# Kernel optimization log

Hardware: AMD Instinct MI355X
Metric: run time of the kernel (lower is better)

Reference implementation:

```python
import jax, jax.numpy as jnp
import numpy as np

# Tree: 64 leaves (16 feat -> 16 out), 8 mids (16 feat + 8*16 child = 144 -> 32 out),
# root (16 feat + 8*32 child = 272 -> 64 out), head -> 10 tasks. Eval-mode BatchNorm.
B = 16384
EPS = 1e-5


def setup_inputs() -> dict:
    key = jax.random.key(0)
    ks = jax.random.split(key, 24)
    rn = lambda k, s: jax.random.normal(k, s, dtype=jnp.float32)
    ru = lambda k, s: jax.random.uniform(k, s, dtype=jnp.float32)
    return {
        "x": rn(ks[0], (B, 1168)),
        # leaf layers (64 nodes, 16 -> 16)
        "Wl": rn(ks[1], (64, 16, 16)) * 0.1, "bl": rn(ks[2], (64, 16)) * 0.1,
        "gl": ru(ks[3], (64, 16)) + 0.5, "betal": rn(ks[4], (64, 16)) * 0.1,
        "ml": rn(ks[5], (64, 16)) * 0.1, "vl": ru(ks[6], (64, 16)) + 0.5,
        # mid layers (8 nodes, 144 -> 32)
        "Wm": rn(ks[7], (8, 144, 32)) * 0.1, "bm": rn(ks[8], (8, 32)) * 0.1,
        "gm": ru(ks[9], (8, 32)) + 0.5, "betam": rn(ks[10], (8, 32)) * 0.1,
        "mm": rn(ks[11], (8, 32)) * 0.1, "vm": ru(ks[12], (8, 32)) + 0.5,
        # root layer (272 -> 64)
        "Wr": rn(ks[13], (272, 64)) * 0.1, "br": rn(ks[14], (64,)) * 0.1,
        "gr": ru(ks[15], (64,)) + 0.5, "betar": rn(ks[16], (64,)) * 0.1,
        "mr": rn(ks[17], (64,)) * 0.1, "vr": ru(ks[18], (64,)) + 0.5,
        # root prediction head (64 -> 10 tasks)
        "Wh": rn(ks[19], (64, 10)) * 0.1, "bh": rn(ks[20], (10,)) * 0.1,
    }


def _bn(h, g, b, m, v):
    return (h - m) * jax.lax.rsqrt(v + EPS) * g + b


def reference(x, Wl, bl, gl, betal, ml, vl, Wm, bm, gm, betam, mm, vm,
              Wr, br, gr, betar, mr, vr, Wh, bh):
    n = x.shape[0]
    # leaves: gather own features (contiguous layout), Linear+BN+Tanh, batched over 64 nodes
    xl = x[:, :1024].reshape(n, 64, 16)
    hl = jnp.tanh(_bn(jnp.einsum('bli,lio->blo', xl, Wl) + bl, gl, betal, ml, vl))
    # mids: concat own features with 8 leaf-child outputs -> [n, 8, 144]
    xm = x[:, 1024:1152].reshape(n, 8, 16)
    mid_in = jnp.concatenate([xm, hl.reshape(n, 8, 128)], axis=-1)
    hm = jnp.tanh(_bn(jnp.einsum('bmi,mio->bmo', mid_in, Wm) + bm, gm, betam, mm, vm))
    # root: concat own features with 8 mid outputs -> [n, 272]
    root_in = jnp.concatenate([x[:, 1152:1168], hm.reshape(n, 256)], axis=-1)
    hr = jnp.tanh(_bn(root_in @ Wr + br, gr, betar, mr, vr))
    # root prediction head (eval-mode forward returns only root prediction)
    return hr @ Wh + bh
```

## Files before the change

kernel.cpp:

```cpp
#include <hip/hip_runtime.h>

typedef __attribute__((ext_vector_type(8))) short bf16x8;
typedef __attribute__((ext_vector_type(4))) float f32x4;

#define EPS 1e-5f

#define N_FRAG_BLOCKS 182
#define WSB_LEAF 0
#define WSB_MID  64
#define WSB_ROOT 144
#define WSB_HEAD 180
#define ST_SL 0
#define ST_TL 1024
#define ST_SM 2048
#define ST_TM 2304
#define ST_SR 2560
#define ST_TR 2624
#define WS_ST_BYTE_OFF (N_FRAG_BLOCKS * 1024)

__device__ __forceinline__ unsigned short f2bf(float f) {
    unsigned u = __float_as_uint(f);
    unsigned r = u + 0x7fffu + ((u >> 16) & 1u);
    return (unsigned short)(r >> 16);
}

__device__ __forceinline__ unsigned pack2bf(float a, float b) {
    return (unsigned)f2bf(a) | ((unsigned)f2bf(b) << 16);
}

__device__ __forceinline__ bf16x8 pack8(float4 a, float4 b) {
    union { unsigned u[4]; bf16x8 v; } r;
    r.u[0] = pack2bf(a.x, a.y); r.u[1] = pack2bf(a.z, a.w);
    r.u[2] = pack2bf(b.x, b.y); r.u[3] = pack2bf(b.z, b.w);
    return r.v;
}

__device__ __forceinline__ float tanh_fast(float x) {
    float e = __expf(2.0f * x);
    return 1.0f - 2.0f / (e + 1.0f);
}

__global__ void ontology_prep(
    const float* __restrict__ Wl, const float* __restrict__ Wm,
    const float* __restrict__ Wr, const float* __restrict__ Wh,
    const float* __restrict__ bl, const float* __restrict__ gl,
    const float* __restrict__ betal, const float* __restrict__ ml,
    const float* __restrict__ vl,
    const float* __restrict__ bm, const float* __restrict__ gm,
    const float* __restrict__ betam, const float* __restrict__ mm,
    const float* __restrict__ vm,
    const float* __restrict__ br, const float* __restrict__ gr,
    const float* __restrict__ betar, const float* __restrict__ mr,
    const float* __restrict__ vr,
    unsigned short* __restrict__ wsFrag, float* __restrict__ wsST)
{
    const int b = blockIdx.x;
    const int t = threadIdx.x;
    if (b < N_FRAG_BLOCKS) {
        const int row = t & 15, g = t >> 4;
        unsigned short vals[8];
        #pragma unroll
        for (int i = 0; i < 8; ++i) {
            const int k = g * 8 + i;
            float v = 0.f;
            if (b < 64) {
                const int l = b;
                if ((l & 1) == 0) { if (k < 16)  v = Wl[l * 256 + k * 16 + row]; }
                else              { if (k >= 16) v = Wl[l * 256 + (k - 16) * 16 + row]; }
            } else if (b < 144) {
                const int idx = b - 64, m = idx / 10, rem = idx % 10;
                const int tt = rem / 5, s = rem % 5;
                const int krow = s * 32 + k;
                if (krow < 144) v = Wm[m * 4608 + krow * 32 + tt * 16 + row];
            } else if (b < 180) {
                const int idx = b - 144, tt = idx / 9, s = idx % 9;
                if (s == 0) { if (k < 16) v = Wr[k * 64 + tt * 16 + row]; }
                else { const int krow = 16 + (s - 1) * 32 + k;
                       v = Wr[krow * 64 + tt * 16 + row]; }
            } else {
                const int s = b - 180, krow = s * 32 + k;
                if (row < 10) v = Wh[krow * 10 + row];
            }
            vals[i] = f2bf(v);
        }
        #pragma unroll
        for (int i = 0; i < 8; ++i) wsFrag[b * 512 + t * 8 + i] = vals[i];
    } else if (b == N_FRAG_BLOCKS) {
        for (int i = 0; i < 16; ++i) {
            const int id = t + 64 * i;
            const float S = gl[id] * rsqrtf(vl[id] + EPS);
            wsST[ST_SL + id] = S;
            wsST[ST_TL + id] = (bl[id] - ml[id]) * S + betal[id];
        }
    } else if (b == N_FRAG_BLOCKS + 1) {
        for (int i = 0; i < 4; ++i) {
            const int id = t + 64 * i;
            const float S = gm[id] * rsqrtf(vm[id] + EPS);
            wsST[ST_SM + id] = S;
            wsST[ST_TM + id] = (bm[id] - mm[id]) * S + betam[id];
        }
    } else {
        const int id = t;
        const float S = gr[id] * rsqrtf(vr[id] + EPS);
        wsST[ST_SR + id] = S;
        wsST[ST_TR + id] = (br[id] - mr[id]) * S + betar[id];
    }
}

__global__ __launch_bounds__(256, 4) void ontology_mfma(
    const float* __restrict__ x,
    const unsigned short* __restrict__ wsFrag,
    const float* __restrict__ wsST,
    const float* __restrict__ bh,
    float* __restrict__ out)
{
    __shared__ __align__(16) unsigned short mid_in[4][16][168];
    __shared__ __align__(16) unsigned short hm[16][264];
    unsigned short (*hr)[72] = (unsigned short (*)[72])&mid_in[0][0][0];

    const int w    = threadIdx.x >> 6;
    const int lane = threadIdx.x & 63;
    const int c    = lane & 15;
    const int g    = lane >> 4;
    const int rowbase = blockIdx.x * 16;
    const float* xrow = x + (size_t)(rowbase + c) * 1168;
    const int m0 = 2 * w, m1 = 2 * w + 1;

    float4 xr_a = *(const float4*)(xrow + 1152 + (g & 1) * 8);
    float4 xr_b = *(const float4*)(xrow + 1152 + (g & 1) * 8 + 4);
    float4 xm4_0 = *(const float4*)(xrow + 1024 + m0 * 16 + 4 * g);
    float4 xm4_1 = *(const float4*)(xrow + 1024 + m1 * 16 + 4 * g);
    float4 xp0[4][2], xp1[4][2];
    #pragma unroll
    for (int p = 0; p < 4; ++p) {
        const float* a0 = xrow + (m0 * 4 + p) * 32 + g * 8;
        xp0[p][0] = *(const float4*)a0;
        xp0[p][1] = *(const float4*)(a0 + 4);
    }
    #pragma unroll
    for (int p = 0; p < 4; ++p) {
        const float* a1 = xrow + (m1 * 4 + p) * 32 + g * 8;
        xp1[p][0] = *(const float4*)a1;
        xp1[p][1] = *(const float4*)(a1 + 4);
    }

    const float* Sl = wsST + ST_SL; const float* Tl = wsST + ST_TL;
    const float* Sm = wsST + ST_SM; const float* Tm = wsST + ST_TM;
    const float* Sr = wsST + ST_SR; const float* Tr = wsST + ST_TR;

    {
        uint2 z; z.x = 0u; z.y = 0u;
        *(uint2*)&mid_in[w][c][144 + 4 * g] = z;
    }

    f32x4 accR;
    {
        bf16x8 bfrag = pack8(xr_a, xr_b);
        bf16x8 a = *(const bf16x8*)(wsFrag + (WSB_ROOT + w * 9) * 512 + lane * 8);
        f32x4 zz = {0.f, 0.f, 0.f, 0.f};
        accR = __builtin_amdgcn_mfma_f32_16x16x32_bf16(a, bfrag, zz, 0, 0, 0);
    }

    auto phase = [&](int mi, const float4& xm4, const float4 xp[4][2]) {
        {
            uint2 pm; pm.x = pack2bf(xm4.x, xm4.y); pm.y = pack2bf(xm4.z, xm4.w);
            *(uint2*)&mid_in[w][c][4 * g] = pm;
        }
        #pragma unroll
        for (int p = 0; p < 4; ++p) {
            bf16x8 bfrag = pack8(xp[p][0], xp[p][1]);
            #pragma unroll
            for (int e = 0; e < 2; ++e) {
                const int leaf = mi * 8 + p * 2 + e;
                bf16x8 afrag = *(const bf16x8*)(wsFrag + (WSB_LEAF + leaf) * 512 + lane * 8);
                f32x4 zz = {0.f, 0.f, 0.f, 0.f};
                f32x4 acc = __builtin_amdgcn_mfma_f32_16x16x32_bf16(afrag, bfrag, zz, 0, 0, 0);
                float4 S = *(const float4*)(Sl + leaf * 16 + 4 * g);
                float4 T = *(const float4*)(Tl + leaf * 16 + 4 * g);
                float h0 = tanh_fast(acc[0] * S.x + T.x);
                float h1 = tanh_fast(acc[1] * S.y + T.y);
                float h2 = tanh_fast(acc[2] * S.z + T.z);
                float h3 = tanh_fast(acc[3] * S.w + T.w);
                uint2 pk; pk.x = pack2bf(h0, h1); pk.y = pack2bf(h2, h3);
                *(uint2*)&mid_in[w][c][16 + (p * 2 + e) * 16 + 4 * g] = pk;
            }
        }
        {
            f32x4 acc0 = {0.f, 0.f, 0.f, 0.f};
            f32x4 acc1 = {0.f, 0.f, 0.f, 0.f};
            const unsigned short* fb = wsFrag + (WSB_MID + mi * 10) * 512 + lane * 8;
            #pragma unroll
            for (int s = 0; s < 5; ++s) {
                bf16x8 bfrag = *(const bf16x8*)&mid_in[w][c][s * 32 + g * 8];
                bf16x8 a0 = *(const bf16x8*)(fb + s * 512);
                bf16x8 a1 = *(const bf16x8*)(fb + (5 + s) * 512);
                acc0 = __builtin_amdgcn_mfma_f32_16x16x32_bf16(a0, bfrag, acc0, 0, 0, 0);
                acc1 = __builtin_amdgcn_mfma_f32_16x16x32_bf16(a1, bfrag, acc1, 0, 0, 0);
            }
            #pragma unroll
            for (int t = 0; t < 2; ++t) {
                f32x4 acc = t ? acc1 : acc0;
                const int po = mi * 32 + t * 16 + 4 * g;
                float4 S = *(const float4*)(Sm + po);
                float4 T = *(const float4*)(Tm + po);
                float h0 = tanh_fast(acc[0] * S.x + T.x);
                float h1 = tanh_fast(acc[1] * S.y + T.y);
                float h2 = tanh_fast(acc[2] * S.z + T.z);
                float h3 = tanh_fast(acc[3] * S.w + T.w);
                uint2 pk; pk.x = pack2bf(h0, h1); pk.y = pack2bf(h2, h3);
                *(uint2*)&hm[c][po] = pk;
            }
        }
    };

    phase(m0, xm4_0, xp0);
    phase(m1, xm4_1, xp1);

    __syncthreads();

    {
        const unsigned short* fb = wsFrag + (WSB_ROOT + w * 9) * 512 + lane * 8;
        #pragma unroll
        for (int s = 1; s <= 8; ++s) {
            bf16x8 bfrag = *(const bf16x8*)&hm[c][(s - 1) * 32 + g * 8];
            bf16x8 a0 = *(const bf16x8*)(fb + s * 512);
            accR = __builtin_amdgcn_mfma_f32_16x16x32_bf16(a0, bfrag, accR, 0, 0, 0);
        }
        const int po = w * 16 + 4 * g;
        float4 S = *(const float4*)(Sr + po);
        float4 T = *(const float4*)(Tr + po);
        float h0 = tanh_fast(accR[0] * S.x + T.x);
        float h1 = tanh_fast(accR[1] * S.y + T.y);
        float h2 = tanh_fast(accR[2] * S.z + T.z);
        float h3 = tanh_fast(accR[3] * S.w + T.w);
        uint2 pk; pk.x = pack2bf(h0, h1); pk.y = pack2bf(h2, h3);
        *(uint2*)&hr[c][po] = pk;
    }
    __syncthreads();

    if (w == 0) {
        f32x4 acc = {0.f, 0.f, 0.f, 0.f};
        #pragma unroll
        for (int s = 0; s < 2; ++s) {
            bf16x8 bfrag = *(const bf16x8*)&hr[c][s * 32 + g * 8];
            bf16x8 a0 = *(const bf16x8*)(wsFrag + (WSB_HEAD + s) * 512 + lane * 8);
            acc = __builtin_amdgcn_mfma_f32_16x16x32_bf16(a0, bfrag, acc, 0, 0, 0);
        }
        float* op = out + (size_t)(rowbase + c) * 10 + 4 * g;
        if (g < 2) {
            float2 o1 = {acc[0] + bh[4 * g],     acc[1] + bh[4 * g + 1]};
            float2 o2 = {acc[2] + bh[4 * g + 2], acc[3] + bh[4 * g + 3]};
            *(float2*)op = o1;
            *(float2*)(op + 2) = o2;
        } else if (g == 2) {
            float2 o1 = {acc[0] + bh[8], acc[1] + bh[9]};
            *(float2*)op = o1;
        }
    }
}

extern "C" void kernel_launch(void* const* d_in, const int* in_sizes, int n_in,
                              void* d_out, int out_size, void* d_ws, size_t ws_size,
                              hipStream_t stream) {
    const float* x     = (const float*)d_in[0];
    const float* Wl    = (const float*)d_in[1];
    const float* bl    = (const float*)d_in[2];
    const float* gl    = (const float*)d_in[3];
    const float* betal = (const float*)d_in[4];
    const float* ml    = (const float*)d_in[5];
    const float* vl    = (const float*)d_in[6];
    const float* Wm    = (const float*)d_in[7];
    const float* bm    = (const float*)d_in[8];
    const float* gm    = (const float*)d_in[9];
    const float* betam = (const float*)d_in[10];
    const float* mm    = (const float*)d_in[11];
    const float* vm    = (const float*)d_in[12];
    const float* Wr    = (const float*)d_in[13];
    const float* br    = (const float*)d_in[14];
    const float* gr    = (const float*)d_in[15];
    const float* betar = (const float*)d_in[16];
    const float* mr    = (const float*)d_in[17];
    const float* vr    = (const float*)d_in[18];
    const float* Wh    = (const float*)d_in[19];
    const float* bh    = (const float*)d_in[20];
    float* out = (float*)d_out;

    unsigned short* wsFrag = (unsigned short*)d_ws;
    float* wsST = (float*)((char*)d_ws + WS_ST_BYTE_OFF);

    ontology_prep<<<N_FRAG_BLOCKS + 3, 64, 0, stream>>>(
        Wl, Wm, Wr, Wh, bl, gl, betal, ml, vl, bm, gm, betam, mm, vm,
        br, gr, betar, mr, vr, wsFrag, wsST);

    const int n = in_sizes[0] / 1168;
    ontology_mfma<<<n / 16, 256, 0, stream>>>(x, wsFrag, wsST, bh, out);
}
```

Baseline: 34.21 us.

## Stage x through LDS with async global_load_lds double buffering and interleaved mids

Replaces per-thread register loads of x with direct global-to-LDS async copies (XOR-swizzled), double-buffered per mid node so the next chunk loads while the current leaves and mid are computed. Work is redistributed so all four waves compute leaves for one mid at a time, two waves compute that mid's output, and the root accumulation is interleaved into the loop. BN scale and shift are prescaled by 2/ln2 so tanh becomes exp2 plus a hardware reciprocal. The change adds many barriers per block and a longer serial chain of eight steps in exchange for coalesced loads and overlap.

```diff
diff --git a/kernel.cpp b/kernel.cpp
--- a/kernel.cpp
+++ b/kernel.cpp
@@ -4,6 +4,7 @@
 typedef __attribute__((ext_vector_type(4))) float f32x4;
 
 #define EPS 1e-5f
+#define K2L 2.8853900817779268f
 
 #define N_FRAG_BLOCKS 182
 #define WSB_LEAF 0
@@ -35,10 +36,20 @@
     return r.v;
 }
 
-__device__ __forceinline__ float tanh_fast(float x) {
-    float e = __expf(2.0f * x);
-    return 1.0f - 2.0f / (e + 1.0f);
-}
+__device__ __forceinline__ float bn_act(float acc, float Sp, float Tp) {
+    float e = exp2f(fmaf(acc, Sp, Tp));
+    float r = __builtin_amdgcn_rcpf(e + 1.0f);
+    return fmaf(-2.0f, r, 1.0f);
+}
+
+__device__ __forceinline__ void gl_lds16(const float* g, float* l) {
+    __builtin_amdgcn_global_load_lds(
+        (const __attribute__((address_space(1))) unsigned int*)g,
+        (__attribute__((address_space(3))) unsigned int*)l, 16, 0, 0);
+}
+
+#define FENCE() asm volatile("" ::: "memory")
+#define BARRIER() do { FENCE(); __builtin_amdgcn_s_barrier(); FENCE(); } while (0)
 
 __global__ void ontology_prep(
     const float* __restrict__ Wl, const float* __restrict__ Wm,
@@ -89,21 +100,21 @@
         for (int i = 0; i < 16; ++i) {
             const int id = t + 64 * i;
             const float S = gl[id] * rsqrtf(vl[id] + EPS);
-            wsST[ST_SL + id] = S;
-            wsST[ST_TL + id] = (bl[id] - ml[id]) * S + betal[id];
+            wsST[ST_SL + id] = S * K2L;
+            wsST[ST_TL + id] = ((bl[id] - ml[id]) * S + betal[id]) * K2L;
         }
     } else if (b == N_FRAG_BLOCKS + 1) {
         for (int i = 0; i < 4; ++i) {
             const int id = t + 64 * i;
             const float S = gm[id] * rsqrtf(vm[id] + EPS);
-            wsST[ST_SM + id] = S;
-            wsST[ST_TM + id] = (bm[id] - mm[id]) * S + betam[id];
+            wsST[ST_SM + id] = S * K2L;
+            wsST[ST_TM + id] = ((bm[id] - mm[id]) * S + betam[id]) * K2L;
         }
     } else {
         const int id = t;
         const float S = gr[id] * rsqrtf(vr[id] + EPS);
-        wsST[ST_SR + id] = S;
-        wsST[ST_TR + id] = (br[id] - mr[id]) * S + betar[id];
+        wsST[ST_SR + id] = S * K2L;
+        wsST[ST_TR + id] = ((br[id] - mr[id]) * S + betar[id]) * K2L;
     }
 }
 
@@ -114,129 +125,157 @@
     const float* __restrict__ bh,
     float* __restrict__ out)
 {
-    __shared__ __align__(16) unsigned short mid_in[4][16][168];
-    __shared__ __align__(16) unsigned short hm[16][264];
-    unsigned short (*hr)[72] = (unsigned short (*)[72])&mid_in[0][0][0];
-
-    const int w    = threadIdx.x >> 6;
-    const int lane = threadIdx.x & 63;
+    __shared__ __align__(16) float xbuf[2][2048];
+    __shared__ __align__(16) float xtail[2304];
+    __shared__ __align__(16) unsigned short mid_in[16][168];
+    __shared__ __align__(16) unsigned short hm[2][16][40];
+    unsigned short (*hr)[72] = (unsigned short (*)[72])&xbuf[0][0];
+
+    const int tid  = threadIdx.x;
+    const int w    = tid >> 6;
+    const int lane = tid & 63;
     const int c    = lane & 15;
     const int g    = lane >> 4;
     const int rowbase = blockIdx.x * 16;
-    const float* xrow = x + (size_t)(rowbase + c) * 1168;
-    const int m0 = 2 * w, m1 = 2 * w + 1;
-
-    float4 xr_a = *(const float4*)(xrow + 1152 + (g & 1) * 8);
-    float4 xr_b = *(const float4*)(xrow + 1152 + (g & 1) * 8 + 4);
-    float4 xm4_0 = *(const float4*)(xrow + 1024 + m0 * 16 + 4 * g);
-    float4 xm4_1 = *(const float4*)(xrow + 1024 + m1 * 16 + 4 * g);
-    float4 xp0[4][2], xp1[4][2];
-    #pragma unroll
-    for (int p = 0; p < 4; ++p) {
-        const float* a0 = xrow + (m0 * 4 + p) * 32 + g * 8;
-        xp0[p][0] = *(const float4*)a0;
-        xp0[p][1] = *(const float4*)(a0 + 4);
-    }
-    #pragma unroll
-    for (int p = 0; p < 4; ++p) {
-        const float* a1 = xrow + (m1 * 4 + p) * 32 + g * 8;
-        xp1[p][0] = *(const float4*)a1;
-        xp1[p][1] = *(const float4*)(a1 + 4);
-    }
+    const float* xbase = x + (size_t)rowbase * 1168;
 
     const float* Sl = wsST + ST_SL; const float* Tl = wsST + ST_TL;
     const float* Sm = wsST + ST_SM; const float* Tm = wsST + ST_TM;
     const float* Sr = wsST + ST_SR; const float* Tr = wsST + ST_TR;
 
-    {
+    int offk[2];
+    #pragma unroll
+    for (int i = 0; i < 2; ++i) {
+        const int k = w * 2 + i;
+        const int row = 2 * k + (lane >> 5);
+        const int gc = (lane & 31) ^ (row & 7);
+        offk[i] = row * 1168 + gc * 4;
+    }
+
+    auto stage = [&](int mm) {
+        const float* bm_ = xbase + mm * 128;
+        float* db = &xbuf[mm & 1][(w * 2) * 256];
+        gl_lds16(bm_ + offk[0], db);
+        gl_lds16(bm_ + offk[1], db + 256);
+    };
+
+    if (w == 1) {
         uint2 z; z.x = 0u; z.y = 0u;
-        *(uint2*)&mid_in[w][c][144 + 4 * g] = z;
-    }
+        *(uint2*)&mid_in[c][144 + 4 * g] = z;
+    }
+
+    #pragma unroll
+    for (int i = 0; i < 2; ++i) {
+        const int kk = w + 4 * i;
+        const int gi = kk * 64 + lane;
+        const int row = gi / 36, col = gi - row * 36;
+        gl_lds16(xbase + row * 1168 + 1024 + col * 4, &xtail[kk * 256]);
+    }
+    if (w == 0) {
+        const int gi = 8 * 64 + lane;
+        const int row = gi / 36, col = gi - row * 36;
+        gl_lds16(xbase + row * 1168 + 1024 + col * 4, &xtail[8 * 256]);
+    }
+    stage(0);
+    stage(1);
+    asm volatile("s_waitcnt vmcnt(2) lgkmcnt(0)" ::: "memory");
+    BARRIER();
 
     f32x4 accR;
     {
-        bf16x8 bfrag = pack8(xr_a, xr_b);
+        const float* rp = &xtail[(c * 36 + 32 + 2 * (g & 1)) * 4];
+        float4 xa = *(const float4*)rp;
+        float4 xb = *(const float4*)(rp + 4);
+        bf16x8 bfrag = pack8(xa, xb);
         bf16x8 a = *(const bf16x8*)(wsFrag + (WSB_ROOT + w * 9) * 512 + lane * 8);
         f32x4 zz = {0.f, 0.f, 0.f, 0.f};
         accR = __builtin_amdgcn_mfma_f32_16x16x32_bf16(a, bfrag, zz, 0, 0, 0);
     }
 
-    auto phase = [&](int mi, const float4& xm4, const float4 xp[4][2]) {
+    #pragma unroll 1
+    for (int m = 0; m < 8; ++m) {
+        if (m > 0) {
+            bf16x8 bfrag = *(const bf16x8*)&hm[(m - 1) & 1][c][g * 8];
+            bf16x8 a = *(const bf16x8*)(wsFrag + (WSB_ROOT + w * 9 + m) * 512 + lane * 8);
+            accR = __builtin_amdgcn_mfma_f32_16x16x32_bf16(a, bfrag, accR, 0, 0, 0);
+        }
         {
-            uint2 pm; pm.x = pack2bf(xm4.x, xm4.y); pm.y = pack2bf(xm4.z, xm4.w);
-            *(uint2*)&mid_in[w][c][4 * g] = pm;
-        }
-        #pragma unroll
-        for (int p = 0; p < 4; ++p) {
-            bf16x8 bfrag = pack8(xp[p][0], xp[p][1]);
+            const float* xb_ = &xbuf[m & 1][0];
+            const int G0 = w * 8 + g * 2;
+            float4 xa = *(const float4*)(xb_ + (c * 32 + (G0 ^ (c & 7))) * 4);
+            float4 x2 = *(const float4*)(xb_ + (c * 32 + ((G0 + 1) ^ (c & 7))) * 4);
+            bf16x8 bfrag = pack8(xa, x2);
             #pragma unroll
             for (int e = 0; e < 2; ++e) {
-                const int leaf = mi * 8 + p * 2 + e;
+                const int leaf = m * 8 + 2 * w + e;
                 bf16x8 afrag = *(const bf16x8*)(wsFrag + (WSB_LEAF + leaf) * 512 + lane * 8);
                 f32x4 zz = {0.f, 0.f, 0.f, 0.f};
                 f32x4 acc = __builtin_amdgcn_mfma_f32_16x16x32_bf16(afrag, bfrag, zz, 0, 0, 0);
-                float4 S = *(const float4*)(Sl + leaf * 16 + 4 * g);
-                float4 T = *(const float4*)(Tl + leaf * 16 + 4 * g);
-                float h0 = tanh_fast(acc[0] * S.x + T.x);
-                float h1 = tanh_fast(acc[1] * S.y + T.y);
-                float h2 = tanh_fast(acc[2] * S.z + T.z);
-                float h3 = tanh_fast(acc[3] * S.w + T.w);
+                const int po = leaf * 16 + 4 * g;
+                float4 S = *(const float4*)(Sl + po);
+                float4 T = *(const float4*)(Tl + po);
+                float h0 = bn_act(acc[0], S.x, T.x);
+                float h1 = bn_act(acc[1], S.y, T.y);
+                float h2 = bn_act(acc[2], S.z, T.z);
+                float h3 = bn_act(acc[3], S.w, T.w);
                 uint2 pk; pk.x = pack2bf(h0, h1); pk.y = pack2bf(h2, h3);
-                *(uint2*)&mid_in[w][c][16 + (p * 2 + e) * 16 + 4 * g] = pk;
+                *(uint2*)&mid_in[c][16 + (2 * w + e) * 16 + 4 * g] = pk;
             }
         }
-        {
-            f32x4 acc0 = {0.f, 0.f, 0.f, 0.f};
-            f32x4 acc1 = {0.f, 0.f, 0.f, 0.f};
-            const unsigned short* fb = wsFrag + (WSB_MID + mi * 10) * 512 + lane * 8;
+        if (w == 0) {
+            const float* xmp = &xtail[(c * 36 + m * 4 + g) * 4];
+            float4 xm4 = *(const float4*)xmp;
+            uint2 pm; pm.x = pack2bf(xm4.x, xm4.y); pm.y = pack2bf(xm4.z, xm4.w);
+            *(uint2*)&mid_in[c][4 * g] = pm;
+        }
+        asm volatile("s_waitcnt lgkmcnt(0)" ::: "memory");
+        BARRIER();
+
+        if (m + 2 < 8) stage(m + 2);
+
+        if (w >= 2) {
+            const int tt = w - 2;
+            f32x4 acc = {0.f, 0.f, 0.f, 0.f};
+            const unsigned short* fb =
+                wsFrag + (WSB_MID + m * 10 + tt * 5) * 512 + lane * 8;
             #pragma unroll
             for (int s = 0; s < 5; ++s) {
-                bf16x8 bfrag = *(const bf16x8*)&mid_in[w][c][s * 32 + g * 8];
+                bf16x8 bfrag = *(const bf16x8*)&mid_in[c][s * 32 + g * 8];
                 bf16x8 a0 = *(const bf16x8*)(fb + s * 512);
-                bf16x8 a1 = *(const bf16x8*)(fb + (5 + s) * 512);
-                acc0 = __builtin_amdgcn_mfma_f32_16x16x32_bf16(a0, bfrag, acc0, 0, 0, 0);
-                acc1 = __builtin_amdgcn_mfma_f32_16x16x32_bf16(a1, bfrag, acc1, 0, 0, 0);
+                acc = __builtin_amdgcn_mfma_f32_16x16x32_bf16(a0, bfrag, acc, 0, 0, 0);
             }
-            #pragma unroll
-            for (int t = 0; t < 2; ++t) {
-                f32x4 acc = t ? acc1 : acc0;
-                const int po = mi * 32 + t * 16 + 4 * g;
-                float4 S = *(const float4*)(Sm + po);
-                float4 T = *(const float4*)(Tm + po);
-                float h0 = tanh_fast(acc[0] * S.x + T.x);
-                float h1 = tanh_fast(acc[1] * S.y + T.y);
-                float h2 = tanh_fast(acc[2] * S.z + T.z);
-                float h3 = tanh_fast(acc[3] * S.w + T.w);
-                uint2 pk; pk.x = pack2bf(h0, h1); pk.y = pack2bf(h2, h3);
-                *(uint2*)&hm[c][po] = pk;
-            }
-        }
-    };
-
-    phase(m0, xm4_0, xp0);
-    phase(m1, xm4_1, xp1);
-
-    __syncthreads();
+            const int po = m * 32 + tt * 16 + 4 * g;
+            float4 S = *(const float4*)(Sm + po);
+            float4 T = *(const float4*)(Tm + po);
+            float h0 = bn_act(acc[0], S.x, T.x);
+            float h1 = bn_act(acc[1], S.y, T.y);
+            float h2 = bn_act(acc[2], S.z, T.z);
+            float h3 = bn_act(acc[3], S.w, T.w);
+            uint2 pk; pk.x = pack2bf(h0, h1); pk.y = pack2bf(h2, h3);
+            *(uint2*)&hm[m & 1][c][tt * 16 + 4 * g] = pk;
+        }
+        if (m < 6) { asm volatile("s_waitcnt vmcnt(2)" ::: "memory"); }
+        else       { asm volatile("s_waitcnt vmcnt(0)" ::: "memory"); }
+        asm volatile("s_waitcnt lgkmcnt(0)" ::: "memory");
+        BARRIER();
+    }
 
     {
-        const unsigned short* fb = wsFrag + (WSB_ROOT + w * 9) * 512 + lane * 8;
-        #pragma unroll
-        for (int s = 1; s <= 8; ++s) {
-            bf16x8 bfrag = *(const bf16x8*)&hm[c][(s - 1) * 32 + g * 8];
-            bf16x8 a0 = *(const bf16x8*)(fb + s * 512);
-            accR = __builtin_amdgcn_mfma_f32_16x16x32_bf16(a0, bfrag, accR, 0, 0, 0);
-        }
+        bf16x8 bfrag = *(const bf16x8*)&hm[1][c][g * 8];
+        bf16x8 a = *(const bf16x8*)(wsFrag + (WSB_ROOT + w * 9 + 8) * 512 + lane * 8);
+        accR = __builtin_amdgcn_mfma_f32_16x16x32_bf16(a, bfrag, accR, 0, 0, 0);
         const int po = w * 16 + 4 * g;
         float4 S = *(const float4*)(Sr + po);
         float4 T = *(const float4*)(Tr + po);
-        float h0 = tanh_fast(accR[0] * S.x + T.x);
-        float h1 = tanh_fast(accR[1] * S.y + T.y);
-        float h2 = tanh_fast(accR[2] * S.z + T.z);
-        float h3 = tanh_fast(accR[3] * S.w + T.w);
+        float h0 = bn_act(accR[0], S.x, T.x);
+        float h1 = bn_act(accR[1], S.y, T.y);
+        float h2 = bn_act(accR[2], S.z, T.z);
+        float h3 = bn_act(accR[3], S.w, T.w);
         uint2 pk; pk.x = pack2bf(h0, h1); pk.y = pack2bf(h2, h3);
         *(uint2*)&hr[c][po] = pk;
     }
-    __syncthreads();
+    asm volatile("s_waitcnt lgkmcnt(0)" ::: "memory");
+    BARRIER();
 
     if (w == 0) {
         f32x4 acc = {0.f, 0.f, 0.f, 0.f};
```

After: 37.68 us. 1.1x slower.
